# Kernel tuning notes

Hardware: AMD Instinct MI355X
Metric: run time of the kernel (lower is better)

The kernel has to match this reference:

```python
import jax, jax.numpy as jnp
import numpy as np

N, M, FEAT, GROUP, EMB = 512, 2048, 1024, 16, 64
DG = FEAT // GROUP  # 64 dims per head


def _make_boxes(k, n):
    k1, k2, k3, k4 = jax.random.split(k, 4)
    x = jax.random.uniform(k1, (n, 1)) * 800.0
    y = jax.random.uniform(k2, (n, 1)) * 800.0
    w = jax.random.uniform(k3, (n, 1)) * 120.0 + 16.0
    h = jax.random.uniform(k4, (n, 1)) * 120.0 + 16.0
    return jnp.concatenate([x, y, x + w, y + h], axis=1)


def setup_inputs() -> dict:
    key = jax.random.key(0)
    ks = jax.random.split(key, 10)
    std = 0.01
    fan = 1.0 / np.sqrt(FEAT).astype(np.float32)
    return {
        "bbox": _make_boxes(ks[0], N),
        "ref_bbox": _make_boxes(ks[1], M),
        "roi_feat": jax.random.normal(ks[2], (N, FEAT), dtype=jnp.float32),
        "ref_feat": jax.random.normal(ks[3], (M, FEAT), dtype=jnp.float32),
        "Wg_w": jax.random.normal(ks[4], (GROUP, EMB)) * std,
        "Wg_b": jnp.zeros((GROUP,), jnp.float32),
        "Wq_w": jax.random.normal(ks[5], (FEAT, FEAT)) * fan,
        "Wq_b": jnp.zeros((FEAT,), jnp.float32),
        "Wk_w": jax.random.normal(ks[6], (FEAT, FEAT)) * fan,
        "Wk_b": jnp.zeros((FEAT,), jnp.float32),
        "Wv_w": jax.random.normal(ks[7], (GROUP, DG, FEAT)) * std,
        "Wv_b": jnp.zeros((FEAT,), jnp.float32),
        "u": jax.random.normal(ks[8], (GROUP, 1, EMB)) * std,
    }


def _position_embedding(bbox, ref_bbox, feat_dim=64, wave_length=1000.0):
    # extract_position_matrix: geometry deltas between every (roi, ref) pair
    xr0, yr0, xr1, yr1 = jnp.split(ref_bbox, 4, axis=1)  # [M,1]
    wr = xr1 - xr0 + 1.0
    hr = yr1 - yr0 + 1.0
    cxr = 0.5 * (xr0 + xr1)
    cyr = 0.5 * (yr0 + yr1)
    x0, y0, x1, y1 = jnp.split(bbox, 4, axis=1)  # [N,1]
    w = x1 - x0 + 1.0
    h = y1 - y0 + 1.0
    cx = 0.5 * (x0 + x1)
    cy = 0.5 * (y0 + y1)
    dx = jnp.log(jnp.abs((cx - cxr.T) / w) + 1e-3)  # [N,M]
    dy = jnp.log(jnp.abs((cy - cyr.T) / h) + 1e-3)
    dw = jnp.log(w / wr.T)
    dh = jnp.log(h / hr.T)
    pos = jnp.stack([dx, dy, dw, dh], axis=2)  # [N,M,4]
    # extract_position_embedding: sinusoidal encoding, feat_dim/8 frequencies
    fr = jnp.arange(feat_dim // 8, dtype=pos.dtype)
    dim_mat = wave_length ** (8.0 / feat_dim * fr)  # [8]
    div = (pos[..., None] * 100.0) / dim_mat  # [N,M,4,8]
    emb = jnp.concatenate([jnp.sin(div), jnp.cos(div)], axis=3)  # [N,M,4,16]
    emb = emb.reshape(emb.shape[0], emb.shape[1], -1)  # [N,M,64]
    return jnp.transpose(emb, (2, 0, 1))  # [emb_dim, N, M]


def reference(bbox, ref_bbox, roi_feat, ref_feat, Wg_w, Wg_b, Wq_w, Wq_b,
              Wk_w, Wk_b, Wv_w, Wv_b, u):
    pe = _position_embedding(bbox, ref_bbox)  # [EMB, N, M]
    # Wg: 1x1 conv over embedding channels, relu -> attention prior weights
    pos_feat = jax.nn.relu(jnp.einsum('ge,enm->gnm', Wg_w, pe)
                           + Wg_b[:, None, None])  # [G,N,M]
    aff_weight = jnp.transpose(pos_feat, (1, 0, 2))  # [N,G,M]
    q = (roi_feat @ Wq_w.T + Wq_b).reshape(-1, GROUP, DG).transpose(1, 0, 2)  # [G,N,DG]
    k = (ref_feat @ Wk_w.T + Wk_b).reshape(-1, GROUP, DG).transpose(1, 0, 2)  # [G,M,DG]
    # content score + global content-bias (u) score, per head
    aff = jnp.einsum('gnd,gmd->gnm', q, k) + jnp.einsum('gld,gmd->glm', u, k)
    aff_scale = (aff / np.sqrt(float(DG))).transpose(1, 0, 2)  # [N,G,M]
    weighted_aff = jnp.log(aff_weight + 1e-6) + aff_scale
    attn = jax.nn.softmax(weighted_aff, axis=2)  # [N,G,M]
    out_t = jnp.einsum('ngm,mf->ngf', attn, ref_feat)  # [N,G,FEAT]
    # grouped 1x1 conv Wv: per-group weight [DG, FEAT]
    out = jnp.einsum('ngc,gdc->ngd', out_t, Wv_w).reshape(-1, FEAT) + Wv_b
    return out  # [N, FEAT]
```

## Files before the change

### kernel.cpp

```cpp
#include <hip/hip_runtime.h>
#include <stdint.h>

typedef float f32x4 __attribute__((ext_vector_type(4)));
typedef _Float16 f16x8 __attribute__((ext_vector_type(8)));
typedef _Float16 f16x4 __attribute__((ext_vector_type(4)));
typedef int int4v __attribute__((ext_vector_type(4)));

#define LOG2E 1.44269504088896340736f

__device__ __forceinline__ void gload_lds16(const void* g, void* l) {
    auto gp = reinterpret_cast<const uint32_t __attribute__((address_space(1)))*>(
        reinterpret_cast<uintptr_t>(g));
    auto lp = reinterpret_cast<uint32_t __attribute__((address_space(3)))*>(
        reinterpret_cast<uintptr_t>(l));
    __builtin_amdgcn_global_load_lds(gp, lp, 16, 0, 0);
}

__global__ __launch_bounds__(256) void mega_prep(
    const float* __restrict__ bbox, const float* __restrict__ ref_bbox,
    const float* __restrict__ roi_feat, const float* __restrict__ ref_feat,
    const float* __restrict__ Wg_w, const float* __restrict__ Wq_w,
    const float* __restrict__ Wk_w, const float* __restrict__ Wv_w,
    const float* __restrict__ Wq_b, const float* __restrict__ uvec,
    _Float16* __restrict__ roi_h, _Float16* __restrict__ ref_h,
    _Float16* __restrict__ wq_h, _Float16* __restrict__ wk_h,
    _Float16* __restrict__ wv_h, _Float16* __restrict__ wg_h,
    float* __restrict__ qbias, float* __restrict__ roig, float* __restrict__ refg)
{
    int idx = blockIdx.x * 256 + threadIdx.x;
    if (idx < 1442048) {
        const float* src; _Float16* dst; int off;
        if (idx < 131072)       { src = roi_feat; dst = roi_h; off = idx; }
        else if (idx < 655360)  { src = ref_feat; dst = ref_h; off = idx - 131072; }
        else if (idx < 917504)  { src = Wq_w;     dst = wq_h;  off = idx - 655360; }
        else if (idx < 1179648) { src = Wk_w;     dst = wk_h;  off = idx - 917504; }
        else if (idx < 1441792) { src = Wv_w;     dst = wv_h;  off = idx - 1179648; }
        else                    { src = Wg_w;     dst = wg_h;  off = idx - 1441792; }
        f32x4 v = *(const f32x4*)(src + (size_t)off * 4);
        f16x4 o;
        o[0] = (_Float16)v[0]; o[1] = (_Float16)v[1];
        o[2] = (_Float16)v[2]; o[3] = (_Float16)v[3];
        *(f16x4*)(dst + (size_t)off * 4) = o;
    } else if (idx < 1442304) {
        int off = idx - 1442048;
        f32x4 a = *(const f32x4*)(Wq_b + off * 4);
        f32x4 b = *(const f32x4*)(uvec + off * 4);
        f32x4 r = a + b;
        *(f32x4*)(qbias + off * 4) = r;
    } else if (idx < 1442816) {
        int n = idx - 1442304;
        f32x4 bb = *(const f32x4*)(bbox + n * 4);
        float w = bb[2] - bb[0] + 1.0f, h = bb[3] - bb[1] + 1.0f;
        f32x4 o1 = {0.5f*(bb[0]+bb[2]), 0.5f*(bb[1]+bb[3]), 1.0f/w, 1.0f/h};
        f32x4 o2 = {__logf(w), __logf(h), 0.f, 0.f};
        *(f32x4*)(roig + n*8) = o1;
        *(f32x4*)(roig + n*8 + 4) = o2;
    } else if (idx < 1444864) {
        int m = idx - 1442816;
        f32x4 bb = *(const f32x4*)(ref_bbox + m * 4);
        float w = bb[2] - bb[0] + 1.0f, h = bb[3] - bb[1] + 1.0f;
        f32x4 o = {0.5f*(bb[0]+bb[2]), 0.5f*(bb[1]+bb[3]), __logf(w), __logf(h)};
        *(f32x4*)(refg + m*4) = o;
    }
}

__global__ __launch_bounds__(256) void mega_gemm(
    const _Float16* __restrict__ roi_h, const _Float16* __restrict__ ref_h,
    const _Float16* __restrict__ wq_h, const _Float16* __restrict__ wk_h,
    const _Float16* __restrict__ wv_h, const float* __restrict__ qbias,
    const float* __restrict__ Wk_b,
    _Float16* __restrict__ Qg, _Float16* __restrict__ Kg, _Float16* __restrict__ Vth)
{
    __shared__ __align__(16) _Float16 As[2][64 * 64];
    __shared__ __align__(16) _Float16 Bs[2][128 * 64];

    int b = blockIdx.x;
    const _Float16 *A, *B;
    const float* bias;
    _Float16* out;
    int tm, tn, mode, MR; float scale;
    if (b < 64)       { A = roi_h; B = wq_h; bias = qbias; out = Qg;  tm = b >> 3;        tn = b & 7;       mode = 0; MR = 512;  scale = 0.125f * LOG2E; }
    else if (b < 320) { A = ref_h; B = wk_h; bias = Wk_b;  out = Kg;  tm = (b-64) >> 3;   tn = (b-64) & 7;  mode = 0; MR = 2048; scale = 1.f; }
    else              { A = ref_h; B = wv_h; bias = nullptr; out = Vth; tm = (b-320) >> 3; tn = (b-320) & 7; mode = 1; MR = 2048; scale = 1.f; }

    int tid = threadIdx.x;
    int w = tid >> 6, l = tid & 63, q = l >> 4, t = l & 15;
    int wm = w >> 1, wn = w & 1;
    int m0 = tm * 64, n0 = tn * 128;

    int r = tid >> 3, c8 = tid & 7;
    int swz = (c8 * 16) ^ ((r & 7) << 4);
    const char* gA = (const char*)A + (size_t)(m0 + r) * 2048 + swz;
    const char* gB = (const char*)B + (size_t)(n0 + r) * 2048 + swz;
    char* lA = (char*)&As[0][0] + (w * 8) * 128;
    char* lB = (char*)&Bs[0][0] + (w * 8) * 128;

#define GSTAGE(bufi, kt) { \
    size_t ko = (size_t)(kt) * 128; \
    gload_lds16(gA + ko,               lA + (bufi)*8192); \
    gload_lds16(gA + ko + 32*2048,     lA + (bufi)*8192 + 32*128); \
    gload_lds16(gB + ko,               lB + (bufi)*16384); \
    gload_lds16(gB + ko + 32*2048,     lB + (bufi)*16384 + 32*128); \
    gload_lds16(gB + ko + 64*2048,     lB + (bufi)*16384 + 64*128); \
    gload_lds16(gB + ko + 96*2048,     lB + (bufi)*16384 + 96*128); }

    f32x4 acc[2][4];
    #pragma unroll
    for (int i = 0; i < 2; ++i)
        #pragma unroll
        for (int j = 0; j < 4; ++j)
            acc[i][j] = (f32x4){0.f, 0.f, 0.f, 0.f};

    GSTAGE(0, 0);
    __syncthreads();

    for (int kt = 0; kt < 16; ++kt) {
        int cur = kt & 1;
        if (kt < 15) GSTAGE(cur ^ 1, kt + 1);

        const char* cA = (const char*)&As[0][0] + cur * 8192;
        const char* cB = (const char*)&Bs[0][0] + cur * 16384;
        f16x8 af[2][2], bf[2][4];
        #pragma unroll
        for (int mi = 0; mi < 2; ++mi) {
            int row = wm * 32 + mi * 16 + t;
            int sx = (row & 7) << 4;
            #pragma unroll
            for (int ks = 0; ks < 2; ++ks)
                af[ks][mi] = *(const f16x8*)(cA + row * 128 + ((ks * 64 + q * 16) ^ sx));
        }
        #pragma unroll
        for (int ni = 0; ni < 4; ++ni) {
            int row = wn * 64 + ni * 16 + t;
            int sx = (row & 7) << 4;
            #pragma unroll
            for (int ks = 0; ks < 2; ++ks)
                bf[ks][ni] = *(const f16x8*)(cB + row * 128 + ((ks * 64 + q * 16) ^ sx));
        }
        #pragma unroll
        for (int ks = 0; ks < 2; ++ks)
            #pragma unroll
            for (int mi = 0; mi < 2; ++mi)
                #pragma unroll
                for (int ni = 0; ni < 4; ++ni)
                    acc[mi][ni] = __builtin_amdgcn_mfma_f32_16x16x32_f16(af[ks][mi], bf[ks][ni], acc[mi][ni], 0, 0, 0);
        __syncthreads();
    }
#undef GSTAGE

    #pragma unroll
    for (int mi = 0; mi < 2; ++mi) {
        #pragma unroll
        for (int ni = 0; ni < 4; ++ni) {
            int col  = n0 + wn*64 + ni*16 + t;
            int row0 = m0 + wm*32 + mi*16 + q*4;
            f32x4 a = acc[mi][ni];
            if (mode == 0) {
                float bb = bias[col];
                _Float16* op = out + ((size_t)(col >> 6) * MR + row0) * 64 + (col & 63);
                #pragma unroll
                for (int rr = 0; rr < 4; ++rr)
                    op[(size_t)rr * 64] = (_Float16)((a[rr] + bb) * scale);
            } else {
                f16x4 pk;
                pk[0] = (_Float16)a[0]; pk[1] = (_Float16)a[1];
                pk[2] = (_Float16)a[2]; pk[3] = (_Float16)a[3];
                *(f16x4*)(out + (size_t)col * 2048 + row0) = pk;
            }
        }
    }
}

__global__ __launch_bounds__(256) void mega_prior(
    const _Float16* __restrict__ wg_h, const float* __restrict__ Wg_b,
    const float* __restrict__ roig, const float* __restrict__ refg,
    _Float16* __restrict__ prior)
{
    int tid = threadIdx.x;
    int w = tid >> 6, l = tid & 63, q = l >> 4, p = l & 15;
    int n = blockIdx.x >> 1, half = blockIdx.x & 1;

    f16x8 wa0 = *(const f16x8*)(wg_h + p*64 + q*8);
    f16x8 wa1 = *(const f16x8*)(wg_h + p*64 + 32 + q*8);
    f32x4 wb = *(const f32x4*)(Wg_b + q*4);

    f32x4 rg1 = *(const f32x4*)(roig + n*8);
    f32x4 rg2 = *(const f32x4*)(roig + n*8 + 4);

    float cf[8];
    #pragma unroll
    for (int f = 0; f < 8; ++f)
        cf[f] = 15.9154943091895336f * __builtin_exp2f(-1.24572303558276059f * (float)f);

    float coff = (q & 1) ? 0.25f : 0.0f;
    bool isX = (q < 2);

    int mstart = half * 1024 + w * 256;
    for (int it = 0; it < 16; ++it) {
        int m = mstart + it * 16 + p;
        f32x4 rg = *(const f32x4*)(refg + m * 4);
        float posA = isX ? __logf(fabsf(rg1[0] - rg[0]) * rg1[2] + 1e-3f)
                         : __logf(fabsf(rg1[1] - rg[1]) * rg1[3] + 1e-3f);
        float posB = isX ? (rg2[0] - rg[2]) : (rg2[1] - rg[3]);
        f16x8 e0, e1;
        #pragma unroll
        for (int f = 0; f < 8; ++f) {
            float a0 = posA * cf[f] + coff; a0 -= floorf(a0);
            float a1 = posB * cf[f] + coff; a1 -= floorf(a1);
            e0[f] = (_Float16)__builtin_amdgcn_sinf(a0);
            e1[f] = (_Float16)__builtin_amdgcn_sinf(a1);
        }
        f32x4 acc = wb;
        acc = __builtin_amdgcn_mfma_f32_16x16x32_f16(wa0, e0, acc, 0, 0, 0);
        acc = __builtin_amdgcn_mfma_f32_16x16x32_f16(wa1, e1, acc, 0, 0, 0);
        _Float16* pp = prior + (size_t)n * 2048 + m;
        #pragma unroll
        for (int r = 0; r < 4; ++r)
            pp[(size_t)(q*4 + r) * 1048576] = (_Float16)fmaxf(acc[r], 0.f);
    }
}

#define SWZ(row, cb) ((cb) ^ (((row) & 7) << 4))

__device__ __forceinline__ f16x8 ld128s(const _Float16* base, int row, int cb) {
    return *(const f16x8*)((const char*)base + row * 128 + SWZ(row, cb));
}
__device__ __forceinline__ f16x4 ld64s(const _Float16* base, int row, int cb) {
    return *(const f16x4*)((const char*)base + row * 128 + SWZ(row, cb));
}

__global__ __launch_bounds__(256, 3) void mega_attn(
    const _Float16* __restrict__ Qg, const _Float16* __restrict__ Kg,
    const _Float16* __restrict__ Vth, const _Float16* __restrict__ prior,
    _Float16* __restrict__ Opart, float* __restrict__ Mpart, float* __restrict__ Lpart)
{
    __shared__ __align__(16) _Float16 Kl[2][4096];
    __shared__ __align__(16) _Float16 Vl[2][4096];
    __shared__ __align__(16) _Float16 Pl[2][4096];

    int bid = blockIdx.x;
    int g = bid >> 6, nt4 = (bid >> 3) & 7, s = bid & 7;
    int tid = threadIdx.x;
    int w = tid >> 6, l = tid & 63, q = l >> 4, t = l & 15;
    int n0 = nt4 * 64, m0 = s * 256;

    int n = n0 + w * 16 + t;
    const _Float16* Qrow = Qg + ((size_t)g * 512 + n) * 64;
    f16x8 qf0 = *(const f16x8*)(Qrow + q * 8);
    f16x8 qf1 = *(const f16x8*)(Qrow + 32 + q * 8);

    int r_lo = tid >> 3, c8 = tid & 7;
    const char* gK = (const char*)(Kg + ((size_t)g * 2048 + m0) * 64);
    const char* gV = (const char*)(Vth + (size_t)g * 64 * 2048 + m0);
    const char* gP = (const char*)(prior + ((size_t)g * 512 + n0) * 2048 + m0);

    int4v kr0, kr1, vr0, vr1, pq0, pq1;
#define LOADC(c) { \
    kr0 = *(const int4v*)(gK + (c)*8192 + r_lo*128 + c8*16); \
    kr1 = *(const int4v*)(gK + (c)*8192 + (r_lo+32)*128 + c8*16); \
    vr0 = *(const int4v*)(gV + (c)*128 + (size_t)r_lo*4096 + c8*16); \
    vr1 = *(const int4v*)(gV + (c)*128 + (size_t)(r_lo+32)*4096 + c8*16); \
    pq0 = *(const int4v*)(gP + (c)*128 + (size_t)r_lo*4096 + c8*16); \
    pq1 = *(const int4v*)(gP + (c)*128 + (size_t)(r_lo+32)*4096 + c8*16); }
#define WRITEC(bufi) { \
    int cb = c8 * 16, sw = SWZ(r_lo, cb); \
    *(int4v*)((char*)&Kl[bufi][0] + r_lo*128 + sw) = kr0; \
    *(int4v*)((char*)&Kl[bufi][0] + (r_lo+32)*128 + sw) = kr1; \
    *(int4v*)((char*)&Vl[bufi][0] + r_lo*128 + sw) = vr0; \
    *(int4v*)((char*)&Vl[bufi][0] + (r_lo+32)*128 + sw) = vr1; \
    *(int4v*)((char*)&Pl[bufi][0] + r_lo*128 + sw) = pq0; \
    *(int4v*)((char*)&Pl[bufi][0] + (r_lo+32)*128 + sw) = pq1; }

    float mrow = -INFINITY, lsum = 0.f;
    f32x4 O0 = {0,0,0,0}, O1 = {0,0,0,0}, O2 = {0,0,0,0}, O3 = {0,0,0,0};

    LOADC(0);
    WRITEC(0);
    __syncthreads();

    for (int c = 0; c < 4; ++c) {
        int cur = c & 1;
        if (c < 3) LOADC(c + 1);

        const _Float16* Kb_l = &Kl[cur][0];
        const _Float16* Vb_l = &Vl[cur][0];
        const _Float16* Pb_l = &Pl[cur][0];

        f16x4 pr[4];
        #pragma unroll
        for (int mi = 0; mi < 4; ++mi)
            pr[mi] = ld64s(Pb_l, w * 16 + t, mi * 32 + q * 8);
        f32x4 sv[4];
        __builtin_amdgcn_s_setprio(1);
        #pragma unroll
        for (int mi = 0; mi < 4; ++mi) {
            f16x8 k0 = ld128s(Kb_l, mi * 16 + t, q * 16);
            f16x8 k1 = ld128s(Kb_l, mi * 16 + t, 64 + q * 16);
            f32x4 z = {0, 0, 0, 0};
            z = __builtin_amdgcn_mfma_f32_16x16x32_f16(k0, qf0, z, 0, 0, 0);
            z = __builtin_amdgcn_mfma_f32_16x16x32_f16(k1, qf1, z, 0, 0, 0);
            sv[mi] = z;
        }
        __builtin_amdgcn_s_setprio(0);
        #pragma unroll
        for (int mi = 0; mi < 4; ++mi)
            #pragma unroll
            for (int r = 0; r < 4; ++r)
                sv[mi][r] += __log2f((float)pr[mi][r] + 1e-6f);
        f16x4 vv[4][4];
        #pragma unroll
        for (int i = 0; i < 4; ++i)
            #pragma unroll
            for (int mi = 0; mi < 4; ++mi)
                vv[i][mi] = ld64s(Vb_l, i * 16 + t, mi * 32 + q * 8);
        float cmax = -INFINITY;
        #pragma unroll
        for (int mi = 0; mi < 4; ++mi)
            #pragma unroll
            for (int r = 0; r < 4; ++r)
                cmax = fmaxf(cmax, sv[mi][r]);
        cmax = fmaxf(cmax, __shfl_xor(cmax, 16));
        cmax = fmaxf(cmax, __shfl_xor(cmax, 32));
        float mnew = fmaxf(mrow, cmax);
        float corr = __builtin_exp2f(mrow - mnew);
        float psum = 0.f;
        f16x4 pf[4];
        #pragma unroll
        for (int mi = 0; mi < 4; ++mi) {
            #pragma unroll
            for (int r = 0; r < 4; ++r) {
                float pv = __builtin_exp2f(sv[mi][r] - mnew);
                psum += pv;
                pf[mi][r] = (_Float16)pv;
            }
        }
        psum += __shfl_xor(psum, 16);
        psum += __shfl_xor(psum, 32);
        lsum = lsum * corr + psum;
        mrow = mnew;
        O0 *= corr; O1 *= corr; O2 *= corr; O3 *= corr;
        __builtin_amdgcn_s_setprio(1);
        #pragma unroll
        for (int mi = 0; mi < 4; ++mi) {
            O0 = __builtin_amdgcn_mfma_f32_16x16x16f16(vv[0][mi], pf[mi], O0, 0, 0, 0);
            O1 = __builtin_amdgcn_mfma_f32_16x16x16f16(vv[1][mi], pf[mi], O1, 0, 0, 0);
            O2 = __builtin_amdgcn_mfma_f32_16x16x16f16(vv[2][mi], pf[mi], O2, 0, 0, 0);
            O3 = __builtin_amdgcn_mfma_f32_16x16x16f16(vv[3][mi], pf[mi], O3, 0, 0, 0);
        }
        __builtin_amdgcn_s_setprio(0);

        if (c < 3) WRITEC(cur ^ 1);
        __syncthreads();
    }

    int u = ((g * 32 + nt4 * 4 + w) << 3) + s;
    size_t ob = (size_t)(u * 16 + t) * 64;
    f16x4 ph;
#define PK(O) { ph[0]=(_Float16)O[0]; ph[1]=(_Float16)O[1]; ph[2]=(_Float16)O[2]; ph[3]=(_Float16)O[3]; }
    PK(O0) *(f16x4*)(Opart + ob + q*4)      = ph;
    PK(O1) *(f16x4*)(Opart + ob + 16 + q*4) = ph;
    PK(O2) *(f16x4*)(Opart + ob + 32 + q*4) = ph;
    PK(O3) *(f16x4*)(Opart + ob + 48 + q*4) = ph;
#undef PK
    if (q == 0) { Mpart[u*16 + t] = mrow; Lpart[u*16 + t] = lsum; }
#undef LOADC
#undef WRITEC
}

__global__ __launch_bounds__(256) void mega_combine(
    const _Float16* __restrict__ Opart, const float* __restrict__ Mpart,
    const float* __restrict__ Lpart, const float* __restrict__ Wv_b,
    float* __restrict__ outp)
{
    int idx = blockIdx.x * 256 + threadIdx.x;
    int n = idx >> 10, col = idx & 1023;
    int g = col >> 6, d = col & 63;
    int nt = n >> 4, t = n & 15;
    int u0 = ((g * 32 + nt) << 3);
    float ms[8];
    #pragma unroll
    for (int s = 0; s < 8; ++s) ms[s] = Mpart[(u0 + s) * 16 + t];
    float M = ms[0];
    #pragma unroll
    for (int s = 1; s < 8; ++s) M = fmaxf(M, ms[s]);
    float accO = 0.f, accL = 0.f;
    #pragma unroll
    for (int s = 0; s < 8; ++s) {
        float wgt = __builtin_exp2f(ms[s] - M);
        accO += wgt * (float)Opart[(size_t)((u0 + s) * 16 + t) * 64 + d];
        accL += wgt * Lpart[(u0 + s) * 16 + t];
    }
    outp[idx] = accO / accL + Wv_b[col];
}

extern "C" void kernel_launch(void* const* d_in, const int* in_sizes, int n_in,
                              void* d_out, int out_size, void* d_ws, size_t ws_size,
                              hipStream_t stream)
{
    const float* bbox     = (const float*)d_in[0];
    const float* ref_bbox = (const float*)d_in[1];
    const float* roi_feat = (const float*)d_in[2];
    const float* ref_feat = (const float*)d_in[3];
    const float* Wg_w = (const float*)d_in[4];
    const float* Wg_b = (const float*)d_in[5];
    const float* Wq_w = (const float*)d_in[6];
    const float* Wq_b = (const float*)d_in[7];
    const float* Wk_w = (const float*)d_in[8];
    const float* Wk_b = (const float*)d_in[9];
    const float* Wv_w = (const float*)d_in[10];
    const float* Wv_b = (const float*)d_in[11];
    const float* uvec = (const float*)d_in[12];
    float* outp = (float*)d_out;
    char* ws = (char*)d_ws;

    _Float16* prior = (_Float16*)ws;
    _Float16* roi_h = (_Float16*)(ws + 0);
    _Float16* ref_h = (_Float16*)(ws + (1ull<<20));
    _Float16* wq_h  = (_Float16*)(ws + (5ull<<20));
    _Float16* wk_h  = (_Float16*)(ws + (7ull<<20));
    _Float16* wv_h  = (_Float16*)(ws + (9ull<<20));
    size_t b2 = 32ull<<20;
    _Float16* wg_h  = (_Float16*)(ws + b2);
    float* qbias    = (float*)(ws + b2 + 4096);
    float* roig     = (float*)(ws + b2 + 8192);
    float* refg     = (float*)(ws + b2 + 24576);
    _Float16* Qh    = (_Float16*)(ws + b2 + 65536);
    _Float16* Kh    = (_Float16*)(ws + b2 + 65536 + (1ull<<20));
    _Float16* Vth   = (_Float16*)(ws + b2 + 65536 + (5ull<<20));
    _Float16* Opart = (_Float16*)(ws + b2 + 65536 + (9ull<<20));
    float* Mpart    = (float*)(ws + b2 + 65536 + (25ull<<20));
    float* Lpart    = (float*)(ws + b2 + 65536 + (25ull<<20) + 262144);

    mega_prep<<<5644, 256, 0, stream>>>(bbox, ref_bbox, roi_feat, ref_feat,
        Wg_w, Wq_w, Wk_w, Wv_w, Wq_b, uvec,
        roi_h, ref_h, wq_h, wk_h, wv_h, wg_h, qbias, roig, refg);
    mega_gemm<<<576, 256, 0, stream>>>(roi_h, ref_h, wq_h, wk_h, wv_h,
        qbias, Wk_b, Qh, Kh, Vth);
    mega_prior<<<1024, 256, 0, stream>>>(wg_h, Wg_b, roig, refg, prior);
    mega_attn<<<1024, 256, 0, stream>>>(Qh, Kh, Vth, prior, Opart, Mpart, Lpart);
    mega_combine<<<2048, 256, 0, stream>>>(Opart, Mpart, Lpart, Wv_b, outp);
}
```

Measured before the change: 149.8 us.

## Fuse projection GEMMs and positional prior into one kernel with smaller tiles

Merges the Q/K/V projection GEMM and the positional-prior kernel into a single launch, with block ID choosing the role. Box geometry and the Q bias are now computed inline instead of in the prep kernel. GEMM tiles shrink from 64x128 to 64x64 so there are more blocks, and launch bounds now request 4 blocks per SM. The aim is to cut one launch and let the compute-bound prior blocks overlap with the GEMM blocks. In exchange, bbox/log work is recomputed per thread and each GEMM block reuses less data.

```diff
diff --git a/kernel.cpp b/kernel.cpp
--- a/kernel.cpp
+++ b/kernel.cpp
@@ -17,98 +17,128 @@
 }
 
 __global__ __launch_bounds__(256) void mega_prep(
-    const float* __restrict__ bbox, const float* __restrict__ ref_bbox,
     const float* __restrict__ roi_feat, const float* __restrict__ ref_feat,
     const float* __restrict__ Wg_w, const float* __restrict__ Wq_w,
     const float* __restrict__ Wk_w, const float* __restrict__ Wv_w,
-    const float* __restrict__ Wq_b, const float* __restrict__ uvec,
     _Float16* __restrict__ roi_h, _Float16* __restrict__ ref_h,
     _Float16* __restrict__ wq_h, _Float16* __restrict__ wk_h,
-    _Float16* __restrict__ wv_h, _Float16* __restrict__ wg_h,
-    float* __restrict__ qbias, float* __restrict__ roig, float* __restrict__ refg)
+    _Float16* __restrict__ wv_h, _Float16* __restrict__ wg_h)
 {
     int idx = blockIdx.x * 256 + threadIdx.x;
-    if (idx < 1442048) {
-        const float* src; _Float16* dst; int off;
-        if (idx < 131072)       { src = roi_feat; dst = roi_h; off = idx; }
-        else if (idx < 655360)  { src = ref_feat; dst = ref_h; off = idx - 131072; }
-        else if (idx < 917504)  { src = Wq_w;     dst = wq_h;  off = idx - 655360; }
-        else if (idx < 1179648) { src = Wk_w;     dst = wk_h;  off = idx - 917504; }
-        else if (idx < 1441792) { src = Wv_w;     dst = wv_h;  off = idx - 1179648; }
-        else                    { src = Wg_w;     dst = wg_h;  off = idx - 1441792; }
-        f32x4 v = *(const f32x4*)(src + (size_t)off * 4);
-        f16x4 o;
-        o[0] = (_Float16)v[0]; o[1] = (_Float16)v[1];
-        o[2] = (_Float16)v[2]; o[3] = (_Float16)v[3];
-        *(f16x4*)(dst + (size_t)off * 4) = o;
-    } else if (idx < 1442304) {
-        int off = idx - 1442048;
-        f32x4 a = *(const f32x4*)(Wq_b + off * 4);
-        f32x4 b = *(const f32x4*)(uvec + off * 4);
-        f32x4 r = a + b;
-        *(f32x4*)(qbias + off * 4) = r;
-    } else if (idx < 1442816) {
-        int n = idx - 1442304;
-        f32x4 bb = *(const f32x4*)(bbox + n * 4);
-        float w = bb[2] - bb[0] + 1.0f, h = bb[3] - bb[1] + 1.0f;
-        f32x4 o1 = {0.5f*(bb[0]+bb[2]), 0.5f*(bb[1]+bb[3]), 1.0f/w, 1.0f/h};
-        f32x4 o2 = {__logf(w), __logf(h), 0.f, 0.f};
-        *(f32x4*)(roig + n*8) = o1;
-        *(f32x4*)(roig + n*8 + 4) = o2;
-    } else if (idx < 1444864) {
-        int m = idx - 1442816;
-        f32x4 bb = *(const f32x4*)(ref_bbox + m * 4);
-        float w = bb[2] - bb[0] + 1.0f, h = bb[3] - bb[1] + 1.0f;
-        f32x4 o = {0.5f*(bb[0]+bb[2]), 0.5f*(bb[1]+bb[3]), __logf(w), __logf(h)};
-        *(f32x4*)(refg + m*4) = o;
-    }
-}
-
-__global__ __launch_bounds__(256) void mega_gemm(
+    const float* src; _Float16* dst; int off;
+    if (idx < 131072)       { src = roi_feat; dst = roi_h; off = idx; }
+    else if (idx < 655360)  { src = ref_feat; dst = ref_h; off = idx - 131072; }
+    else if (idx < 917504)  { src = Wq_w;     dst = wq_h;  off = idx - 655360; }
+    else if (idx < 1179648) { src = Wk_w;     dst = wk_h;  off = idx - 917504; }
+    else if (idx < 1441792) { src = Wv_w;     dst = wv_h;  off = idx - 1179648; }
+    else                    { src = Wg_w;     dst = wg_h;  off = idx - 1441792; }
+    f32x4 v = *(const f32x4*)(src + (size_t)off * 4);
+    f16x4 o;
+    o[0] = (_Float16)v[0]; o[1] = (_Float16)v[1];
+    o[2] = (_Float16)v[2]; o[3] = (_Float16)v[3];
+    *(f16x4*)(dst + (size_t)off * 4) = o;
+}
+
+__global__ __launch_bounds__(256, 4) void mega_gp(
     const _Float16* __restrict__ roi_h, const _Float16* __restrict__ ref_h,
     const _Float16* __restrict__ wq_h, const _Float16* __restrict__ wk_h,
-    const _Float16* __restrict__ wv_h, const float* __restrict__ qbias,
-    const float* __restrict__ Wk_b,
-    _Float16* __restrict__ Qg, _Float16* __restrict__ Kg, _Float16* __restrict__ Vth)
+    const _Float16* __restrict__ wv_h, const _Float16* __restrict__ wg_h,
+    const float* __restrict__ Wq_b, const float* __restrict__ uvec,
+    const float* __restrict__ Wk_b, const float* __restrict__ Wg_b,
+    const float* __restrict__ bbox, const float* __restrict__ ref_bbox,
+    _Float16* __restrict__ Qg, _Float16* __restrict__ Kg, _Float16* __restrict__ Vth,
+    _Float16* __restrict__ prior)
 {
-    __shared__ __align__(16) _Float16 As[2][64 * 64];
-    __shared__ __align__(16) _Float16 Bs[2][128 * 64];
+    __shared__ __align__(16) _Float16 As[2][4096];
+    __shared__ __align__(16) _Float16 Bs[2][4096];
 
     int b = blockIdx.x;
-    const _Float16 *A, *B;
-    const float* bias;
-    _Float16* out;
-    int tm, tn, mode, MR; float scale;
-    if (b < 64)       { A = roi_h; B = wq_h; bias = qbias; out = Qg;  tm = b >> 3;        tn = b & 7;       mode = 0; MR = 512;  scale = 0.125f * LOG2E; }
-    else if (b < 320) { A = ref_h; B = wk_h; bias = Wk_b;  out = Kg;  tm = (b-64) >> 3;   tn = (b-64) & 7;  mode = 0; MR = 2048; scale = 1.f; }
-    else              { A = ref_h; B = wv_h; bias = nullptr; out = Vth; tm = (b-320) >> 3; tn = (b-320) & 7; mode = 1; MR = 2048; scale = 1.f; }
-
     int tid = threadIdx.x;
     int w = tid >> 6, l = tid & 63, q = l >> 4, t = l & 15;
+
+    if (b >= 1152) {
+        int pb = b - 1152;
+        int p = l & 15;
+        int n = pb >> 1, half = pb & 1;
+
+        f16x8 wa0 = *(const f16x8*)(wg_h + p*64 + q*8);
+        f16x8 wa1 = *(const f16x8*)(wg_h + p*64 + 32 + q*8);
+        f32x4 wb = *(const f32x4*)(Wg_b + q*4);
+
+        f32x4 bbx = *(const f32x4*)(bbox + n * 4);
+        float bw = bbx[2] - bbx[0] + 1.0f, bh = bbx[3] - bbx[1] + 1.0f;
+        float cx = 0.5f*(bbx[0]+bbx[2]), cy = 0.5f*(bbx[1]+bbx[3]);
+        float invw = 1.0f/bw, invh = 1.0f/bh;
+        float lgw = __logf(bw), lgh = __logf(bh);
+
+        float cf[8];
+        #pragma unroll
+        for (int f = 0; f < 8; ++f)
+            cf[f] = 15.9154943091895336f * __builtin_exp2f(-1.24572303558276059f * (float)f);
+
+        float coff = (q & 1) ? 0.25f : 0.0f;
+        bool isX = (q < 2);
+        float cA  = isX ? cx : cy;
+        float invA = isX ? invw : invh;
+        float lgA = isX ? lgw : lgh;
+
+        int mstart = half * 1024 + w * 256;
+        for (int it = 0; it < 16; ++it) {
+            int m = mstart + it * 16 + p;
+            f32x4 rb = *(const f32x4*)(ref_bbox + m * 4);
+            float cAr = isX ? 0.5f*(rb[0]+rb[2]) : 0.5f*(rb[1]+rb[3]);
+            float sAr = isX ? (rb[2]-rb[0]+1.0f) : (rb[3]-rb[1]+1.0f);
+            float posA = __logf(fabsf(cA - cAr) * invA + 1e-3f);
+            float posB = lgA - __logf(sAr);
+            f16x8 e0, e1;
+            #pragma unroll
+            for (int f = 0; f < 8; ++f) {
+                float a0 = posA * cf[f] + coff; a0 -= floorf(a0);
+                float a1 = posB * cf[f] + coff; a1 -= floorf(a1);
+                e0[f] = (_Float16)__builtin_amdgcn_sinf(a0);
+                e1[f] = (_Float16)__builtin_amdgcn_sinf(a1);
+            }
+            f32x4 acc = wb;
+            acc = __builtin_amdgcn_mfma_f32_16x16x32_f16(wa0, e0, acc, 0, 0, 0);
+            acc = __builtin_amdgcn_mfma_f32_16x16x32_f16(wa1, e1, acc, 0, 0, 0);
+            _Float16* pp = prior + (size_t)n * 2048 + m;
+            #pragma unroll
+            for (int r = 0; r < 4; ++r)
+                pp[(size_t)(q*4 + r) * 1048576] = (_Float16)fmaxf(acc[r], 0.f);
+        }
+        return;
+    }
+
+    const _Float16 *A, *B;
+    _Float16* out;
+    int tm, tn, mode; float scale;
+    if (b < 128)      { A = roi_h; B = wq_h; out = Qg;  tm = b >> 4;        tn = b & 15;       mode = 0; scale = 0.125f * LOG2E; }
+    else if (b < 640) { A = ref_h; B = wk_h; out = Kg;  tm = (b-128) >> 4;  tn = (b-128) & 15; mode = 1; scale = 1.f; }
+    else              { A = ref_h; B = wv_h; out = Vth; tm = (b-640) >> 4;  tn = (b-640) & 15; mode = 2; scale = 1.f; }
+    int MR = (b < 128) ? 512 : 2048;
+
     int wm = w >> 1, wn = w & 1;
-    int m0 = tm * 64, n0 = tn * 128;
-
-    int r = tid >> 3, c8 = tid & 7;
-    int swz = (c8 * 16) ^ ((r & 7) << 4);
-    const char* gA = (const char*)A + (size_t)(m0 + r) * 2048 + swz;
-    const char* gB = (const char*)B + (size_t)(n0 + r) * 2048 + swz;
-    char* lA = (char*)&As[0][0] + (w * 8) * 128;
-    char* lB = (char*)&Bs[0][0] + (w * 8) * 128;
+    int m0 = tm * 64, n0 = tn * 64;
+
+    int r_lo = tid >> 3, c8 = tid & 7;
+    int swz = (c8 * 16) ^ ((r_lo & 7) << 4);
+    const char* gA = (const char*)A + (size_t)(m0 + r_lo) * 2048 + swz;
+    const char* gB = (const char*)B + (size_t)(n0 + r_lo) * 2048 + swz;
+    char* lA = (char*)&As[0][0] + w * 1024;
+    char* lB = (char*)&Bs[0][0] + w * 1024;
 
 #define GSTAGE(bufi, kt) { \
     size_t ko = (size_t)(kt) * 128; \
-    gload_lds16(gA + ko,               lA + (bufi)*8192); \
-    gload_lds16(gA + ko + 32*2048,     lA + (bufi)*8192 + 32*128); \
-    gload_lds16(gB + ko,               lB + (bufi)*16384); \
-    gload_lds16(gB + ko + 32*2048,     lB + (bufi)*16384 + 32*128); \
-    gload_lds16(gB + ko + 64*2048,     lB + (bufi)*16384 + 64*128); \
-    gload_lds16(gB + ko + 96*2048,     lB + (bufi)*16384 + 96*128); }
-
-    f32x4 acc[2][4];
+    gload_lds16(gA + ko,           lA + (bufi)*8192); \
+    gload_lds16(gA + ko + 32*2048, lA + (bufi)*8192 + 4096); \
+    gload_lds16(gB + ko,           lB + (bufi)*8192); \
+    gload_lds16(gB + ko + 32*2048, lB + (bufi)*8192 + 4096); }
+
+    f32x4 acc[2][2];
     #pragma unroll
     for (int i = 0; i < 2; ++i)
         #pragma unroll
-        for (int j = 0; j < 4; ++j)
+        for (int j = 0; j < 2; ++j)
             acc[i][j] = (f32x4){0.f, 0.f, 0.f, 0.f};
 
     GSTAGE(0, 0);
@@ -119,8 +149,8 @@
         if (kt < 15) GSTAGE(cur ^ 1, kt + 1);
 
         const char* cA = (const char*)&As[0][0] + cur * 8192;
-        const char* cB = (const char*)&Bs[0][0] + cur * 16384;
-        f16x8 af[2][2], bf[2][4];
+        const char* cB = (const char*)&Bs[0][0] + cur * 8192;
+        f16x8 af[2][2], bf[2][2];
         #pragma unroll
         for (int mi = 0; mi < 2; ++mi) {
             int row = wm * 32 + mi * 16 + t;
@@ -130,8 +160,8 @@
                 af[ks][mi] = *(const f16x8*)(cA + row * 128 + ((ks * 64 + q * 16) ^ sx));
         }
         #pragma unroll
-        for (int ni = 0; ni < 4; ++ni) {
-            int row = wn * 64 + ni * 16 + t;
+        for (int ni = 0; ni < 2; ++ni) {
+            int row = wn * 32 + ni * 16 + t;
             int sx = (row & 7) << 4;
             #pragma unroll
             for (int ks = 0; ks < 2; ++ks)
@@ -142,7 +172,7 @@
             #pragma unroll
             for (int mi = 0; mi < 2; ++mi)
                 #pragma unroll
-                for (int ni = 0; ni < 4; ++ni)
+                for (int ni = 0; ni < 2; ++ni)
                     acc[mi][ni] = __builtin_amdgcn_mfma_f32_16x16x32_f16(af[ks][mi], bf[ks][ni], acc[mi][ni], 0, 0, 0);
         __syncthreads();
     }
@@ -151,72 +181,23 @@
     #pragma unroll
     for (int mi = 0; mi < 2; ++mi) {
         #pragma unroll
-        for (int ni = 0; ni < 4; ++ni) {
-            int col  = n0 + wn*64 + ni*16 + t;
+        for (int ni = 0; ni < 2; ++ni) {
+            int col  = n0 + wn*32 + ni*16 + t;
             int row0 = m0 + wm*32 + mi*16 + q*4;
             f32x4 a = acc[mi][ni];
-            if (mode == 0) {
-                float bb = bias[col];
+            if (mode == 2) {
+                f16x4 pk;
+                pk[0] = (_Float16)a[0]; pk[1] = (_Float16)a[1];
+                pk[2] = (_Float16)a[2]; pk[3] = (_Float16)a[3];
+                *(f16x4*)(out + (size_t)col * 2048 + row0) = pk;
+            } else {
+                float bb = (mode == 0) ? (Wq_b[col] + uvec[col]) : Wk_b[col];
                 _Float16* op = out + ((size_t)(col >> 6) * MR + row0) * 64 + (col & 63);
                 #pragma unroll
                 for (int rr = 0; rr < 4; ++rr)
                     op[(size_t)rr * 64] = (_Float16)((a[rr] + bb) * scale);
-            } else {
-                f16x4 pk;
-                pk[0] = (_Float16)a[0]; pk[1] = (_Float16)a[1];
-                pk[2] = (_Float16)a[2]; pk[3] = (_Float16)a[3];
-                *(f16x4*)(out + (size_t)col * 2048 + row0) = pk;
             }
         }
-    }
-}
-
-__global__ __launch_bounds__(256) void mega_prior(
-    const _Float16* __restrict__ wg_h, const float* __restrict__ Wg_b,
-    const float* __restrict__ roig, const float* __restrict__ refg,
-    _Float16* __restrict__ prior)
-{
-    int tid = threadIdx.x;
-    int w = tid >> 6, l = tid & 63, q = l >> 4, p = l & 15;
-    int n = blockIdx.x >> 1, half = blockIdx.x & 1;
-
-    f16x8 wa0 = *(const f16x8*)(wg_h + p*64 + q*8);
-    f16x8 wa1 = *(const f16x8*)(wg_h + p*64 + 32 + q*8);
-    f32x4 wb = *(const f32x4*)(Wg_b + q*4);
-
-    f32x4 rg1 = *(const f32x4*)(roig + n*8);
-    f32x4 rg2 = *(const f32x4*)(roig + n*8 + 4);
-
-    float cf[8];
-    #pragma unroll
-    for (int f = 0; f < 8; ++f)
-        cf[f] = 15.9154943091895336f * __builtin_exp2f(-1.24572303558276059f * (float)f);
-
-    float coff = (q & 1) ? 0.25f : 0.0f;
-    bool isX = (q < 2);
-
-    int mstart = half * 1024 + w * 256;
-    for (int it = 0; it < 16; ++it) {
-        int m = mstart + it * 16 + p;
-        f32x4 rg = *(const f32x4*)(refg + m * 4);
-        float posA = isX ? __logf(fabsf(rg1[0] - rg[0]) * rg1[2] + 1e-3f)
-                         : __logf(fabsf(rg1[1] - rg[1]) * rg1[3] + 1e-3f);
-        float posB = isX ? (rg2[0] - rg[2]) : (rg2[1] - rg[3]);
-        f16x8 e0, e1;
-        #pragma unroll
-        for (int f = 0; f < 8; ++f) {
-            float a0 = posA * cf[f] + coff; a0 -= floorf(a0);
-            float a1 = posB * cf[f] + coff; a1 -= floorf(a1);
-            e0[f] = (_Float16)__builtin_amdgcn_sinf(a0);
-            e1[f] = (_Float16)__builtin_amdgcn_sinf(a1);
-        }
-        f32x4 acc = wb;
-        acc = __builtin_amdgcn_mfma_f32_16x16x32_f16(wa0, e0, acc, 0, 0, 0);
-        acc = __builtin_amdgcn_mfma_f32_16x16x32_f16(wa1, e1, acc, 0, 0, 0);
-        _Float16* pp = prior + (size_t)n * 2048 + m;
-        #pragma unroll
-        for (int r = 0; r < 4; ++r)
-            pp[(size_t)(q*4 + r) * 1048576] = (_Float16)fmaxf(acc[r], 0.f);
     }
 }
 
@@ -413,30 +394,28 @@
     float* outp = (float*)d_out;
     char* ws = (char*)d_ws;
 
-    _Float16* prior = (_Float16*)ws;
     _Float16* roi_h = (_Float16*)(ws + 0);
     _Float16* ref_h = (_Float16*)(ws + (1ull<<20));
     _Float16* wq_h  = (_Float16*)(ws + (5ull<<20));
     _Float16* wk_h  = (_Float16*)(ws + (7ull<<20));
     _Float16* wv_h  = (_Float16*)(ws + (9ull<<20));
-    size_t b2 = 32ull<<20;
-    _Float16* wg_h  = (_Float16*)(ws + b2);
-    float* qbias    = (float*)(ws + b2 + 4096);
-    float* roig     = (float*)(ws + b2 + 8192);
-    float* refg     = (float*)(ws + b2 + 24576);
-    _Float16* Qh    = (_Float16*)(ws + b2 + 65536);
-    _Float16* Kh    = (_Float16*)(ws + b2 + 65536 + (1ull<<20));
-    _Float16* Vth   = (_Float16*)(ws + b2 + 65536 + (5ull<<20));
-    _Float16* Opart = (_Float16*)(ws + b2 + 65536 + (9ull<<20));
-    float* Mpart    = (float*)(ws + b2 + 65536 + (25ull<<20));
-    float* Lpart    = (float*)(ws + b2 + 65536 + (25ull<<20) + 262144);
-
-    mega_prep<<<5644, 256, 0, stream>>>(bbox, ref_bbox, roi_feat, ref_feat,
-        Wg_w, Wq_w, Wk_w, Wv_w, Wq_b, uvec,
-        roi_h, ref_h, wq_h, wk_h, wv_h, wg_h, qbias, roig, refg);
-    mega_gemm<<<576, 256, 0, stream>>>(roi_h, ref_h, wq_h, wk_h, wv_h,
-        qbias, Wk_b, Qh, Kh, Vth);
-    mega_prior<<<1024, 256, 0, stream>>>(wg_h, Wg_b, roig, refg, prior);
+    _Float16* wg_h  = (_Float16*)(ws + (11ull<<20));
+    size_t b2 = 12ull<<20;
+    _Float16* prior = (_Float16*)(ws + b2);
+    size_t b3 = b2 + (32ull<<20);
+    _Float16* Qh    = (_Float16*)(ws + b3);
+    _Float16* Kh    = (_Float16*)(ws + b3 + (1ull<<20));
+    _Float16* Vth   = (_Float16*)(ws + b3 + (5ull<<20));
+    _Float16* Opart = (_Float16*)(ws + b3 + (9ull<<20));
+    float* Mpart    = (float*)(ws + b3 + (25ull<<20));
+    float* Lpart    = (float*)(ws + b3 + (25ull<<20) + 262144);
+
+    mega_prep<<<5633, 256, 0, stream>>>(roi_feat, ref_feat,
+        Wg_w, Wq_w, Wk_w, Wv_w,
+        roi_h, ref_h, wq_h, wk_h, wv_h, wg_h);
+    mega_gp<<<2176, 256, 0, stream>>>(roi_h, ref_h, wq_h, wk_h, wv_h, wg_h,
+        Wq_b, uvec, Wk_b, Wg_b, bbox, ref_bbox,
+        Qh, Kh, Vth, prior);
     mega_attn<<<1024, 256, 0, stream>>>(Qh, Kh, Vth, prior, Opart, Mpart, Lpart);
     mega_combine<<<2048, 256, 0, stream>>>(Opart, Mpart, Lpart, Wv_b, outp);
 }
```

After: 146.9 us. Within noise of the previous version (-2.0%).
